# Optimization experiments

Measured on AMD Instinct MI355X. Metric: run time of the kernel, lower is better.

The kernel has to match this reference:

```python
import jax, jax.numpy as jnp
import numpy as np

N = 163842          # icosphere level-7 vertex count
IN_FEATS = 64
OUT_FEATS = 64
K = 7               # 1-ring: self + 6 neighbors


def setup_inputs() -> dict:
    key = jax.random.key(0)
    kx, ko, kw, kb = jax.random.split(key, 4)
    x = jax.random.normal(kx, (N, IN_FEATS), dtype=jnp.float32)
    neigh_orders = jax.random.randint(ko, (N * K,), 0, N, dtype=jnp.int64)
    # torch nn.Linear(7*in_feats, out_feats): weight [out, 7*in], bias [out]
    W = jax.random.normal(kw, (OUT_FEATS, K * IN_FEATS), dtype=jnp.float32) * (1.0 / np.sqrt(K * IN_FEATS))
    b = jax.random.normal(kb, (OUT_FEATS,), dtype=jnp.float32) * 0.01
    return {"x": x, "neigh_orders": neigh_orders, "W": W, "b": b}


def reference(x, neigh_orders, W, b):
    n = x.shape[0]
    # gather 7 neighbor feature vectors per node, flatten: [N, 7*in_feats]
    mat = jnp.take(x, neigh_orders, axis=0).reshape(n, K * IN_FEATS)
    # linear layer: [N, 7*in] @ [7*in, out] + [out]
    return mat @ W.T + b
```

## Files before the change

kernel.cpp:

```cpp
#include <hip/hip_runtime.h>
#include <hip/hip_bf16.h>

#define IN_FEATS 64
#define OUT_FEATS 64
#define K_NEIGH 7
#define KDIM (K_NEIGH * IN_FEATS)
#define KSTEPS (KDIM / 32)

typedef __bf16 bf16x8 __attribute__((ext_vector_type(8)));
typedef float  f32x4  __attribute__((ext_vector_type(4)));

__device__ __forceinline__ unsigned short f2bf(float f) {
    union { float f; unsigned int u; } v; v.f = f;
    unsigned int u = v.u;
    unsigned int r = (u + 0x7FFFu + ((u >> 16) & 1u)) >> 16;
    return (unsigned short)r;
}

__global__ __launch_bounds__(256)
void cast_x_bf16(const float* __restrict__ x, __bf16* __restrict__ xb, int total8) {
    int i = blockIdx.x * 256 + threadIdx.x;
    const int stride = gridDim.x * 256;
    for (; i < total8; i += stride) {
        f32x4 a0 = *(const f32x4*)(x + (long)i * 8);
        f32x4 a1 = *(const f32x4*)(x + (long)i * 8 + 4);
        bf16x8 o;
        o[0] = (__bf16)a0.x; o[1] = (__bf16)a0.y; o[2] = (__bf16)a0.z; o[3] = (__bf16)a0.w;
        o[4] = (__bf16)a1.x; o[5] = (__bf16)a1.y; o[6] = (__bf16)a1.z; o[7] = (__bf16)a1.w;
        *(bf16x8*)(xb + (long)i * 8) = o;
    }
}

template<bool PRECAST>
__global__ __launch_bounds__(512, 4)
void onering_mfma2(const float* __restrict__ x,
                   const __bf16* __restrict__ xb,
                   const int*   __restrict__ neigh,
                   const float* __restrict__ W,
                   const float* __restrict__ b,
                   float* __restrict__ out,
                   int n)
{
    __shared__ unsigned short wlds[OUT_FEATS * KDIM];

    const int tid  = threadIdx.x;
    const int wid  = tid >> 6;
    const int lane = tid & 63;
    const int lhi  = lane >> 4;
    const int llo  = lane & 15;

    for (int i = tid; i < (OUT_FEATS * KDIM) / 4; i += 512) {
        f32x4 w4 = *(const f32x4*)(W + i * 4);
        int e   = i * 4;
        int row = e / KDIM;
        ushort4 h;
        h.x = f2bf(w4.x); h.y = f2bf(w4.y); h.z = f2bf(w4.z); h.w = f2bf(w4.w);
        int byteoff = e * 2;
        byteoff ^= ((row & 7) << 4);
        *(ushort4*)((char*)wlds + byteoff) = h;
    }
    __syncthreads();

    const int rowbase = (blockIdx.x * 8 + wid) * 32;

    int nidx[2][K_NEIGH];
    #pragma unroll
    for (int rt = 0; rt < 2; ++rt) {
        int r  = rowbase + rt * 16 + llo;
        int rr = (r < n) ? r : 0;
        #pragma unroll
        for (int kn = 0; kn < K_NEIGH; ++kn)
            nidx[rt][kn] = neigh[(long)rr * K_NEIGH + kn];
    }

    f32x4 acc[2][4] = {};

    #pragma unroll
    for (int kn = 0; kn < K_NEIGH; ++kn) {
        bf16x8 afr[2][2];
        #pragma unroll
        for (int rt = 0; rt < 2; ++rt) {
            const long src = nidx[rt][kn];
            if (PRECAST) {
                const __bf16* xp = xb + src * IN_FEATS + lhi * 8;
                afr[rt][0] = *(const bf16x8*)(xp);
                afr[rt][1] = *(const bf16x8*)(xp + 32);
            } else {
                const float* xp = x + src * IN_FEATS + lhi * 8;
                #pragma unroll
                for (int h = 0; h < 2; ++h) {
                    f32x4 a0 = *(const f32x4*)(xp + h * 32);
                    f32x4 a1 = *(const f32x4*)(xp + h * 32 + 4);
                    bf16x8 af;
                    af[0] = (__bf16)a0.x; af[1] = (__bf16)a0.y;
                    af[2] = (__bf16)a0.z; af[3] = (__bf16)a0.w;
                    af[4] = (__bf16)a1.x; af[5] = (__bf16)a1.y;
                    af[6] = (__bf16)a1.z; af[7] = (__bf16)a1.w;
                    afr[rt][h] = af;
                }
            }
        }

        #pragma unroll
        for (int h = 0; h < 2; ++h) {
            const int kk = kn * 2 + h;
            const int klocal = kk * 32 + lhi * 8;
            bf16x8 bfrag[4];
            #pragma unroll
            for (int ct = 0; ct < 4; ++ct) {
                int ocol    = ct * 16 + llo;
                int byteoff = ocol * (KDIM * 2) + klocal * 2;
                byteoff ^= ((ocol & 7) << 4);
                bfrag[ct] = *(const bf16x8*)((const char*)wlds + byteoff);
            }
            #pragma unroll
            for (int ct = 0; ct < 4; ++ct)
                #pragma unroll
                for (int rt = 0; rt < 2; ++rt)
                    acc[rt][ct] = __builtin_amdgcn_mfma_f32_16x16x32_bf16(
                                      afr[rt][h], bfrag[ct], acc[rt][ct], 0, 0, 0);
        }
    }

    #pragma unroll
    for (int ct = 0; ct < 4; ++ct) {
        float bias = b[ct * 16 + llo];
        #pragma unroll
        for (int rt = 0; rt < 2; ++rt)
            #pragma unroll
            for (int j = 0; j < 4; ++j)
                acc[rt][ct][j] += bias;
    }

    #pragma unroll
    for (int rt = 0; rt < 2; ++rt) {
        const int rbase = rowbase + rt * 16 + lhi * 4;
        #pragma unroll
        for (int j = 0; j < 4; ++j) {
            const int r = rbase + j;
            if (r < n) {
                #pragma unroll
                for (int ct = 0; ct < 4; ++ct)
                    out[(long)r * OUT_FEATS + ct * 16 + llo] = acc[rt][ct][j];
            }
        }
    }
}

extern "C" void kernel_launch(void* const* d_in, const int* in_sizes, int n_in,
                              void* d_out, int out_size, void* d_ws, size_t ws_size,
                              hipStream_t stream) {
    const float* x     = (const float*)d_in[0];
    const int*   neigh = (const int*)d_in[1];
    const float* W     = (const float*)d_in[2];
    const float* b     = (const float*)d_in[3];
    float* out = (float*)d_out;

    const int n = in_sizes[0] / IN_FEATS;
    const int nblocks = (n + 255) / 256;

    const size_t xb_bytes = (size_t)n * IN_FEATS * sizeof(unsigned short);
    if (ws_size >= xb_bytes) {
        __bf16* xb = (__bf16*)d_ws;
        const int total8 = n * IN_FEATS / 8;
        cast_x_bf16<<<dim3(2048), dim3(256), 0, stream>>>(x, xb, total8);
        onering_mfma2<true><<<dim3(nblocks), dim3(512), 0, stream>>>(
            x, xb, neigh, W, b, out, n);
    } else {
        onering_mfma2<false><<<dim3(nblocks), dim3(512), 0, stream>>>(
            x, nullptr, neigh, W, b, out, n);
    }
}
```

Before: 50.84 us.

## Prefetch all neighbor gathers before weight staging barrier in bf16 path

In the precast path, the kernel now loads neighbor indices first and issues every gathered bf16 A-fragment load for all seven neighbors into registers. It does this before the shared-memory weight staging and __syncthreads, so the gather latency overlaps the weight conversion. The cost is many more live registers (28 bf16x8 fragments), so launch bounds drop to 2 blocks per SM, lowering occupancy. The fp32 fallback is split into its own non-template kernel with unchanged logic.

```diff
diff --git a/kernel.cpp b/kernel.cpp
--- a/kernel.cpp
+++ b/kernel.cpp
@@ -5,7 +5,6 @@
 #define OUT_FEATS 64
 #define K_NEIGH 7
 #define KDIM (K_NEIGH * IN_FEATS)
-#define KSTEPS (KDIM / 32)
 
 typedef __bf16 bf16x8 __attribute__((ext_vector_type(8)));
 typedef float  f32x4  __attribute__((ext_vector_type(4)));
@@ -31,10 +30,8 @@
     }
 }
 
-template<bool PRECAST>
-__global__ __launch_bounds__(512, 4)
-void onering_mfma2(const float* __restrict__ x,
-                   const __bf16* __restrict__ xb,
+__global__ __launch_bounds__(512, 2)
+void onering_mfma4(const __bf16* __restrict__ xb,
                    const int*   __restrict__ neigh,
                    const float* __restrict__ W,
                    const float* __restrict__ b,
@@ -48,6 +45,18 @@
     const int lane = tid & 63;
     const int lhi  = lane >> 4;
     const int llo  = lane & 15;
+
+    const int rowbase = (blockIdx.x * 8 + wid) * 32;
+
+    int nidx[2][K_NEIGH];
+    #pragma unroll
+    for (int rt = 0; rt < 2; ++rt) {
+        int r  = rowbase + rt * 16 + llo;
+        int rr = (r < n) ? r : 0;
+        #pragma unroll
+        for (int kn = 0; kn < K_NEIGH; ++kn)
+            nidx[rt][kn] = neigh[(long)rr * K_NEIGH + kn];
+    }
 
     for (int i = tid; i < (OUT_FEATS * KDIM) / 4; i += 512) {
         f32x4 w4 = *(const f32x4*)(W + i * 4);
@@ -59,48 +68,24 @@
         byteoff ^= ((row & 7) << 4);
         *(ushort4*)((char*)wlds + byteoff) = h;
     }
+
+    bf16x8 af[K_NEIGH][2][2];
+    #pragma unroll
+    for (int kn = 0; kn < K_NEIGH; ++kn)
+        #pragma unroll
+        for (int rt = 0; rt < 2; ++rt) {
+            const __bf16* xp = xb + (long)nidx[rt][kn] * IN_FEATS + lhi * 8;
+            af[kn][rt][0] = *(const bf16x8*)(xp);
+            af[kn][rt][1] = *(const bf16x8*)(xp + 32);
+        }
+    __builtin_amdgcn_sched_barrier(0);
+
+    f32x4 acc[2][4] = {};
+
     __syncthreads();
 
-    const int rowbase = (blockIdx.x * 8 + wid) * 32;
-
-    int nidx[2][K_NEIGH];
-    #pragma unroll
-    for (int rt = 0; rt < 2; ++rt) {
-        int r  = rowbase + rt * 16 + llo;
-        int rr = (r < n) ? r : 0;
-        #pragma unroll
-        for (int kn = 0; kn < K_NEIGH; ++kn)
-            nidx[rt][kn] = neigh[(long)rr * K_NEIGH + kn];
-    }
-
-    f32x4 acc[2][4] = {};
-
     #pragma unroll
     for (int kn = 0; kn < K_NEIGH; ++kn) {
-        bf16x8 afr[2][2];
-        #pragma unroll
-        for (int rt = 0; rt < 2; ++rt) {
-            const long src = nidx[rt][kn];
-            if (PRECAST) {
-                const __bf16* xp = xb + src * IN_FEATS + lhi * 8;
-                afr[rt][0] = *(const bf16x8*)(xp);
-                afr[rt][1] = *(const bf16x8*)(xp + 32);
-            } else {
-                const float* xp = x + src * IN_FEATS + lhi * 8;
-                #pragma unroll
-                for (int h = 0; h < 2; ++h) {
-                    f32x4 a0 = *(const f32x4*)(xp + h * 32);
-                    f32x4 a1 = *(const f32x4*)(xp + h * 32 + 4);
-                    bf16x8 af;
-                    af[0] = (__bf16)a0.x; af[1] = (__bf16)a0.y;
-                    af[2] = (__bf16)a0.z; af[3] = (__bf16)a0.w;
-                    af[4] = (__bf16)a1.x; af[5] = (__bf16)a1.y;
-                    af[6] = (__bf16)a1.z; af[7] = (__bf16)a1.w;
-                    afr[rt][h] = af;
-                }
-            }
-        }
-
         #pragma unroll
         for (int h = 0; h < 2; ++h) {
             const int kk = kn * 2 + h;
@@ -118,7 +103,7 @@
                 #pragma unroll
                 for (int rt = 0; rt < 2; ++rt)
                     acc[rt][ct] = __builtin_amdgcn_mfma_f32_16x16x32_bf16(
-                                      afr[rt][h], bfrag[ct], acc[rt][ct], 0, 0, 0);
+                                      af[kn][rt][h], bfrag[ct], acc[rt][ct], 0, 0, 0);
         }
     }
 
@@ -132,6 +117,108 @@
                 acc[rt][ct][j] += bias;
     }
 
+    #pragma unroll
+    for (int rt = 0; rt < 2; ++rt) {
+        const int rbase = rowbase + rt * 16 + lhi * 4;
+        #pragma unroll
+        for (int j = 0; j < 4; ++j) {
+            const int r = rbase + j;
+            if (r < n) {
+                #pragma unroll
+                for (int ct = 0; ct < 4; ++ct)
+                    out[(long)r * OUT_FEATS + ct * 16 + llo] = acc[rt][ct][j];
+            }
+        }
+    }
+}
+
+__global__ __launch_bounds__(512, 4)
+void onering_mfma_f32(const float* __restrict__ x,
+                      const int*   __restrict__ neigh,
+                      const float* __restrict__ W,
+                      const float* __restrict__ b,
+                      float* __restrict__ out,
+                      int n)
+{
+    __shared__ unsigned short wlds[OUT_FEATS * KDIM];
+    const int tid  = threadIdx.x;
+    const int wid  = tid >> 6;
+    const int lane = tid & 63;
+    const int lhi  = lane >> 4;
+    const int llo  = lane & 15;
+
+    for (int i = tid; i < (OUT_FEATS * KDIM) / 4; i += 512) {
+        f32x4 w4 = *(const f32x4*)(W + i * 4);
+        int e   = i * 4;
+        int row = e / KDIM;
+        ushort4 h;
+        h.x = f2bf(w4.x); h.y = f2bf(w4.y); h.z = f2bf(w4.z); h.w = f2bf(w4.w);
+        int byteoff = e * 2;
+        byteoff ^= ((row & 7) << 4);
+        *(ushort4*)((char*)wlds + byteoff) = h;
+    }
+    __syncthreads();
+
+    const int rowbase = (blockIdx.x * 8 + wid) * 32;
+    int nidx[2][K_NEIGH];
+    #pragma unroll
+    for (int rt = 0; rt < 2; ++rt) {
+        int r  = rowbase + rt * 16 + llo;
+        int rr = (r < n) ? r : 0;
+        #pragma unroll
+        for (int kn = 0; kn < K_NEIGH; ++kn)
+            nidx[rt][kn] = neigh[(long)rr * K_NEIGH + kn];
+    }
+
+    f32x4 acc[2][4] = {};
+    #pragma unroll
+    for (int kn = 0; kn < K_NEIGH; ++kn) {
+        bf16x8 afr[2][2];
+        #pragma unroll
+        for (int rt = 0; rt < 2; ++rt) {
+            const float* xp = x + (long)nidx[rt][kn] * IN_FEATS + lhi * 8;
+            #pragma unroll
+            for (int h = 0; h < 2; ++h) {
+                f32x4 a0 = *(const f32x4*)(xp + h * 32);
+                f32x4 a1 = *(const f32x4*)(xp + h * 32 + 4);
+                bf16x8 a;
+                a[0] = (__bf16)a0.x; a[1] = (__bf16)a0.y;
+                a[2] = (__bf16)a0.z; a[3] = (__bf16)a0.w;
+                a[4] = (__bf16)a1.x; a[5] = (__bf16)a1.y;
+                a[6] = (__bf16)a1.z; a[7] = (__bf16)a1.w;
+                afr[rt][h] = a;
+            }
+        }
+        #pragma unroll
+        for (int h = 0; h < 2; ++h) {
+            const int kk = kn * 2 + h;
+            const int klocal = kk * 32 + lhi * 8;
+            bf16x8 bfrag[4];
+            #pragma unroll
+            for (int ct = 0; ct < 4; ++ct) {
+                int ocol    = ct * 16 + llo;
+                int byteoff = ocol * (KDIM * 2) + klocal * 2;
+                byteoff ^= ((ocol & 7) << 4);
+                bfrag[ct] = *(const bf16x8*)((const char*)wlds + byteoff);
+            }
+            #pragma unroll
+            for (int ct = 0; ct < 4; ++ct)
+                #pragma unroll
+                for (int rt = 0; rt < 2; ++rt)
+                    acc[rt][ct] = __builtin_amdgcn_mfma_f32_16x16x32_bf16(
+                                      afr[rt][h], bfrag[ct], acc[rt][ct], 0, 0, 0);
+        }
+    }
+
+    #pragma unroll
+    for (int ct = 0; ct < 4; ++ct) {
+        float bias = b[ct * 16 + llo];
+        #pragma unroll
+        for (int rt = 0; rt < 2; ++rt)
+            #pragma unroll
+            for (int j = 0; j < 4; ++j)
+                acc[rt][ct][j] += bias;
+    }
     #pragma unroll
     for (int rt = 0; rt < 2; ++rt) {
         const int rbase = rowbase + rt * 16 + lhi * 4;
@@ -164,10 +251,10 @@
         __bf16* xb = (__bf16*)d_ws;
         const int total8 = n * IN_FEATS / 8;
         cast_x_bf16<<<dim3(2048), dim3(256), 0, stream>>>(x, xb, total8);
-        onering_mfma2<true><<<dim3(nblocks), dim3(512), 0, stream>>>(
-            x, xb, neigh, W, b, out, n);
+        onering_mfma4<<<dim3(nblocks), dim3(512), 0, stream>>>(
+            xb, neigh, W, b, out, n);
     } else {
-        onering_mfma2<false><<<dim3(nblocks), dim3(512), 0, stream>>>(
-            x, nullptr, neigh, W, b, out, n);
-    }
-}
+        onering_mfma_f32<<<dim3(nblocks), dim3(512), 0, stream>>>(
+            x, neigh, W, b, out, n);
+    }
+}
```

Measured after the change: 57.84 us. 1.14x slower.
